# Performance work log

Hardware: AMD Instinct MI355X
Metric: run time of the kernel (lower is better)

## Reference

```python
import jax, jax.numpy as jnp
import numpy as np

N_COND, K, D = 16, 512, 256
B, H, W = 32, 64, 64


def setup_inputs() -> dict:
    key = jax.random.key(0)
    k1, k2, k3 = jax.random.split(key, 3)
    z_e_x = jax.random.normal(k1, (B, D, H, W), dtype=jnp.float32)
    C = jax.random.randint(k2, (B,), 0, N_COND, dtype=jnp.int64)
    bound = 1.0 / (K * N_COND)
    weight = jax.random.uniform(k3, (N_COND, K, D), dtype=jnp.float32,
                                minval=-bound, maxval=bound)
    return {"z_e_x": z_e_x, "C": C, "weight": weight}


def reference(z_e_x, C, weight):
    b, d, h, w = z_e_x.shape
    # [B, H, W, D] -> [B, N, D] with N = H*W
    z = jnp.transpose(z_e_x, (0, 2, 3, 1)).reshape(b, h * w, d)
    cb = weight[C]  # per-sample codebook [B, K, D] (batched gather replaces python loop)
    # squared euclidean distances: ||z||^2 - 2 z.e + ||e||^2  -> [B, N, K]
    dist = (jnp.sum(z * z, axis=-1, keepdims=True)
            - 2.0 * jnp.einsum('bnd,bkd->bnk', z, cb)
            + jnp.sum(cb * cb, axis=-1)[:, None, :])
    idx = jnp.argmin(dist, axis=-1)  # [B, N]
    quant = jnp.take_along_axis(cb, idx[..., None], axis=1)  # [B, N, D]
    # straight-through output (vq_st): forward = quantized
    z_q = z + jax.lax.stop_gradient(quant - z)
    # z_q_x_bar: plain gather from (non-detached) codebook
    z_q_bar = quant
    z_q_x = jnp.transpose(z_q.reshape(b, h, w, d), (0, 3, 1, 2))
    z_q_x_bar = jnp.transpose(z_q_bar.reshape(b, h, w, d), (0, 3, 1, 2))
    return z_q_x, z_q_x_bar
```

## Files before the change

kernel.cpp:

```cpp
#include <hip/hip_runtime.h>
#include <cfloat>

#define NB    32
#define ND    256
#define NK    512
#define NCOND 16
#define NHW   4096
#define PXT   64
#define MARGIN 1.3e-4f
#define QCAP  16

typedef __attribute__((ext_vector_type(8))) short bf16x8;
typedef __attribute__((ext_vector_type(4))) float f32x4;

__device__ __forceinline__ int loadC(const int* __restrict__ C, int b) {
  int orodd = 0;
#pragma unroll
  for (int i = 1; i < 32; i += 2) orodd |= C[i];
  return (orodd == 0) ? C[2 * b] : C[b];
}

__device__ __forceinline__ unsigned short rne_bf16(float x) {
  unsigned u = __float_as_uint(x);
  u += 0x7fffu + ((u >> 16) & 1u);
  return (unsigned short)(u >> 16);
}

__device__ float np_score_g(const float* __restrict__ z, size_t zoff,
                            const float* __restrict__ er, float S) {
  float P0 = 0.f, P1 = 0.f, P2 = 0.f, P3 = 0.f;
  for (int ch = 0; ch < 16; ++ch) {
    const float* eb = er + ch * 16;
    float4 e0 = *(const float4*)(eb + 0);
    float4 e1 = *(const float4*)(eb + 4);
    float4 e2 = *(const float4*)(eb + 8);
    float4 e3 = *(const float4*)(eb + 12);
    float zb[16];
#pragma unroll
    for (int q = 0; q < 16; ++q)
      zb[q] = z[zoff + (size_t)(ch * 16 + q) * NHW];
    P0 = __fadd_rn(P0, __fmul_rn(zb[12], e3.x));
    P0 = __fadd_rn(P0, __fmul_rn(zb[8],  e2.x));
    P0 = __fadd_rn(P0, __fmul_rn(zb[4],  e1.x));
    P0 = __fadd_rn(P0, __fmul_rn(zb[0],  e0.x));
    P1 = __fadd_rn(P1, __fmul_rn(zb[13], e3.y));
    P1 = __fadd_rn(P1, __fmul_rn(zb[9],  e2.y));
    P1 = __fadd_rn(P1, __fmul_rn(zb[5],  e1.y));
    P1 = __fadd_rn(P1, __fmul_rn(zb[1],  e0.y));
    P2 = __fadd_rn(P2, __fmul_rn(zb[14], e3.z));
    P2 = __fadd_rn(P2, __fmul_rn(zb[10], e2.z));
    P2 = __fadd_rn(P2, __fmul_rn(zb[6],  e1.z));
    P2 = __fadd_rn(P2, __fmul_rn(zb[2],  e0.z));
    P3 = __fadd_rn(P3, __fmul_rn(zb[15], e3.w));
    P3 = __fadd_rn(P3, __fmul_rn(zb[11], e2.w));
    P3 = __fadd_rn(P3, __fmul_rn(zb[7],  e1.w));
    P3 = __fadd_rn(P3, __fmul_rn(zb[3],  e0.w));
  }
  float G = __fadd_rn(__fadd_rn(P0, P1), __fadd_rn(P2, P3));
  return __fadd_rn(S, __fmul_rn(-2.0f, G));
}

__global__ __launch_bounds__(256) void k_split(
    const float* __restrict__ w, unsigned short* __restrict__ whi) {
  int i = (blockIdx.x * 256 + threadIdx.x) * 4;
  float4 v = *(const float4*)&w[i];
  int ci = i >> 17, rem = i & 131071;
  int code = rem >> 8, d = rem & 255;
  int dst = (ci << 17) + ((d >> 5) << 14) + (code << 5) + (d & 31);
  ushort4 h;
  h.x = rne_bf16(v.x); h.y = rne_bf16(v.y);
  h.z = rne_bf16(v.z); h.w = rne_bf16(v.w);
  *(ushort4*)&whi[dst] = h;
}

__device__ __forceinline__ int zofs(int px, int chunk) {
  return px * 256 + ((chunk ^ (px & 7)) * 8);
}

template <int PRE>
__global__ __launch_bounds__(512, 4) void k_vq(
    const float* __restrict__ z, const int* __restrict__ Cc,
    const float* __restrict__ w, const unsigned short* __restrict__ whi,
    float* __restrict__ out) {
  __shared__ __align__(16) unsigned short Zh[PXT * ND];
  __shared__ __align__(16) unsigned short Zl[PXT * ND];
  __shared__ float Ssh[PXT];
  __shared__ float Wmin[8][32];
  __shared__ float Thr[PXT];
  __shared__ int   qcnt[PXT], KB[PXT];
  __shared__ int   qk[PXT][QCAP];

  int orig = blockIdx.x;
  int blk  = (orig & 7) * 256 + (orig >> 3);
  int b    = blk >> 6;
  int n0   = (blk & 63) * PXT;
  int c    = loadC(Cc, b);
  int t    = threadIdx.x;
  int lane = t & 63;
  int wv   = t >> 6;
  int mw   = wv >> 2;
  int nw   = wv & 3;

  if (t < PXT) qcnt[t] = 0;

  const size_t zab = (size_t)b * ND * NHW;
  const size_t cbu = (size_t)c * (NK * ND);
  const int ar0  = mw * 32 + (lane & 15);
  const int koff = (lane >> 4) * 8;

  {
    int px = t & 63, dg = t >> 6;
    const float* zp = z + zab + n0 + px;
#pragma unroll
    for (int cc4 = 0; cc4 < 4; ++cc4) {
      int chunk = dg * 4 + cc4;
      bf16x8 h, l;
#pragma unroll
      for (int j = 0; j < 8; ++j) {
        float v = zp[(size_t)(chunk * 8 + j) * NHW];
        unsigned u = __float_as_uint(v) & 0xffff0000u;
        h[j] = (short)(u >> 16);
        l[j] = (short)rne_bf16(v - __uint_as_float(u));
      }
      *(bf16x8*)&Zh[zofs(px, chunk)] = h;
      *(bf16x8*)&Zl[zofs(px, chunk)] = l;
    }
  }

  {
    int spx = t >> 3, sj = t & 7;
    size_t sb = zab + n0 + spx;
    float r0 = 0.f, r1 = 0.f;
#pragma unroll
    for (int i = 0; i < 16; ++i) {
      float v0 = z[sb + (size_t)(8 * i + sj) * NHW];
      float v1 = z[sb + (size_t)(128 + 8 * i + sj) * NHW];
      r0 = __fadd_rn(r0, __fmul_rn(v0, v0));
      r1 = __fadd_rn(r1, __fmul_rn(v1, v1));
    }
#pragma unroll
    for (int off = 1; off < 8; off <<= 1) {
      r0 = __fadd_rn(r0, __shfl_xor(r0, off));
      r1 = __fadd_rn(r1, __shfl_xor(r1, off));
    }
    if (sj == 0) Ssh[spx] = __fadd_rn(r0, r1);
  }
  __syncthreads();

  f32x4 acc0[8], acc1[8];
#pragma unroll
  for (int nt = 0; nt < 8; ++nt) {
    acc0[nt] = (f32x4){0.f, 0.f, 0.f, 0.f};
    acc1[nt] = (f32x4){0.f, 0.f, 0.f, 0.f};
  }

#pragma unroll 1
  for (int ks = 0; ks < 8; ++ks) {
    int chunkA = ks * 4 + (lane >> 4);
    bf16x8 ah0 = *(const bf16x8*)&Zh[zofs(ar0,      chunkA)];
    bf16x8 al0 = *(const bf16x8*)&Zl[zofs(ar0,      chunkA)];
    bf16x8 ah1 = *(const bf16x8*)&Zh[zofs(ar0 + 16, chunkA)];
    bf16x8 al1 = *(const bf16x8*)&Zl[zofs(ar0 + 16, chunkA)];
#pragma unroll
    for (int nt = 0; nt < 8; ++nt) {
      int code = nw * 128 + nt * 16 + (lane & 15);
      bf16x8 bh;
      if constexpr (PRE) {
        bh = *(const bf16x8*)(whi + cbu + ks * (NK * 32) + code * 32 + koff);
      } else {
        const float* sf = w + ((size_t)c * NK + code) * ND + ks * 32 + koff;
        float4 f0 = *(const float4*)sf;
        float4 f1 = *(const float4*)(sf + 4);
        float xs[8] = {f0.x, f0.y, f0.z, f0.w, f1.x, f1.y, f1.z, f1.w};
#pragma unroll
        for (int q = 0; q < 8; ++q) bh[q] = (short)rne_bf16(xs[q]);
      }
      acc0[nt] = __builtin_amdgcn_mfma_f32_16x16x32_bf16(ah0, bh, acc0[nt], 0, 0, 0);
      acc0[nt] = __builtin_amdgcn_mfma_f32_16x16x32_bf16(al0, bh, acc0[nt], 0, 0, 0);
      acc1[nt] = __builtin_amdgcn_mfma_f32_16x16x32_bf16(ah1, bh, acc1[nt], 0, 0, 0);
      acc1[nt] = __builtin_amdgcn_mfma_f32_16x16x32_bf16(al1, bh, acc1[nt], 0, 0, 0);
    }
  }

  float pmin0[4], pmin1[4], S40[4], S41[4];
#pragma unroll
  for (int r = 0; r < 4; ++r) {
    int pr = mw * 32 + (lane >> 4) * 4 + r;
    S40[r] = Ssh[pr];
    S41[r] = Ssh[pr + 16];
    pmin0[r] = FLT_MAX; pmin1[r] = FLT_MAX;
  }
#pragma unroll
  for (int nt = 0; nt < 8; ++nt)
#pragma unroll
    for (int r = 0; r < 4; ++r) {
      float X0 = __fadd_rn(S40[r], __fmul_rn(-2.0f, acc0[nt][r]));
      float X1 = __fadd_rn(S41[r], __fmul_rn(-2.0f, acc1[nt][r]));
      acc0[nt][r] = X0; acc1[nt][r] = X1;
      pmin0[r] = fminf(pmin0[r], X0);
      pmin1[r] = fminf(pmin1[r], X1);
    }
#pragma unroll
  for (int r = 0; r < 4; ++r)
#pragma unroll
    for (int off = 1; off < 16; off <<= 1) {
      pmin0[r] = fminf(pmin0[r], __shfl_xor(pmin0[r], off));
      pmin1[r] = fminf(pmin1[r], __shfl_xor(pmin1[r], off));
    }
  if ((lane & 15) == 0) {
#pragma unroll
    for (int r = 0; r < 4; ++r) {
      Wmin[wv][(lane >> 4) * 4 + r]      = pmin0[r];
      Wmin[wv][16 + (lane >> 4) * 4 + r] = pmin1[r];
    }
  }
  __syncthreads();
  if (t < PXT) {
    int m2 = (t >> 5) * 4, i = t & 31;
    Thr[t] = fminf(fminf(Wmin[m2][i], Wmin[m2 + 1][i]),
                   fminf(Wmin[m2 + 2][i], Wmin[m2 + 3][i])) + MARGIN;
  }
  __syncthreads();

#pragma unroll
  for (int r = 0; r < 4; ++r) {
    int px0 = mw * 32 + (lane >> 4) * 4 + r;
    float th0 = Thr[px0], th1 = Thr[px0 + 16];
#pragma unroll
    for (int nt = 0; nt < 8; ++nt) {
      int kcode = nw * 128 + nt * 16 + (lane & 15);
      if (acc0[nt][r] <= th0) {
        int slot = atomicAdd(&qcnt[px0], 1);
        if (slot < QCAP) qk[px0][slot] = kcode;
      }
      if (acc1[nt][r] <= th1) {
        int slot = atomicAdd(&qcnt[px0 + 16], 1);
        if (slot < QCAP) qk[px0 + 16][slot] = kcode;
      }
    }
  }
  __syncthreads();

  {
    int px  = wv * 8 + (lane >> 3);
    int cnt = qcnt[px]; cnt = cnt < QCAP ? cnt : QCAP;
    float S = Ssh[px];
    size_t zoff = zab + n0 + px;
    float bv = FLT_MAX; int bk = 0x7fffffff;
#pragma unroll
    for (int m = 0; m < 2; ++m) {
      int slot = (lane & 7) + 8 * m;
      if (__any(slot < cnt)) {
        if (slot < cnt) {
          int k = qk[px][slot];
          float v = np_score_g(z, zoff, w + ((size_t)c * NK + k) * ND, S);
          if (v < bv || (v == bv && k < bk)) { bv = v; bk = k; }
        }
      }
    }
#pragma unroll
    for (int off = 1; off < 8; off <<= 1) {
      float ov = __shfl_xor(bv, off);
      int   ok = __shfl_xor(bk, off);
      if (ov < bv || (ov == bv && ok < bk)) { bv = ov; bk = ok; }
    }
    if ((lane & 7) == 0) KB[px] = bk;
  }
  __syncthreads();

  {
    int px = t & 63, dg = t >> 6;
    int kidx = KB[px];
    const float* er = w + ((size_t)c * NK + kidx) * ND;
    const size_t OUT2 = (size_t)NB * ND * NHW;
    size_t base = zab + n0 + px;
#pragma unroll
    for (int j = 0; j < 32; ++j) {
      int d = dg * 32 + j;
      float q  = er[d];
      float zv = z[base + (size_t)d * NHW];
      out[base + (size_t)d * NHW]        = __fadd_rn(zv, __fsub_rn(q, zv));
      out[base + (size_t)d * NHW + OUT2] = q;
    }
  }
}

extern "C" void kernel_launch(void* const* d_in, const int* in_sizes, int n_in,
                              void* d_out, int out_size, void* d_ws, size_t ws_size,
                              hipStream_t stream) {
  const float* z = (const float*)d_in[0];
  const int*   C = (const int*)d_in[1];
  const float* w = (const float*)d_in[2];
  float* out = (float*)d_out;

  const size_t NWEL = (size_t)NCOND * NK * ND;
  unsigned short* whi = (unsigned short*)d_ws;
  bool pre = ws_size >= NWEL * sizeof(unsigned short);

  if (pre) {
    k_split<<<(int)(NWEL / 1024), 256, 0, stream>>>(w, whi);
    k_vq<1><<<NB * (NHW / PXT), 512, 0, stream>>>(z, C, w, whi, out);
  } else {
    k_vq<0><<<NB * (NHW / PXT), 512, 0, stream>>>(z, C, w, whi, out);
  }
}
```

Before: 233.2 us.

## Split VQ kernel into score and gather kernels, skip rescoring single candidates

Moves the output writing out of the score kernel into a separate gather kernel launched with 256 threads, which reads the codebook row with float4 loads. Indices pass between the two kernels through a workspace buffer. The squared-norm computation now reduces through shared memory instead of shuffles. The refinement pass no longer rescores pixels that have only one candidate. The split lowers register and LDS pressure in the score kernel and frees the store phase from its occupancy limits, at the cost of an extra launch, an index round trip and reading z again. The fallback path now uses the workspace for indices, so it needs workspace memory it did not need before.

```diff
diff --git a/kernel.cpp b/kernel.cpp
--- a/kernel.cpp
+++ b/kernel.cpp
@@ -78,10 +78,10 @@
 }
 
 template <int PRE>
-__global__ __launch_bounds__(512, 4) void k_vq(
+__global__ __launch_bounds__(512, 4) void k_score(
     const float* __restrict__ z, const int* __restrict__ Cc,
     const float* __restrict__ w, const unsigned short* __restrict__ whi,
-    float* __restrict__ out) {
+    int* __restrict__ idxOut) {
   __shared__ __align__(16) unsigned short Zh[PXT * ND];
   __shared__ __align__(16) unsigned short Zl[PXT * ND];
   __shared__ float Ssh[PXT];
@@ -89,6 +89,8 @@
   __shared__ float Thr[PXT];
   __shared__ int   qcnt[PXT], KB[PXT];
   __shared__ int   qk[PXT][QCAP];
+
+  float* Rsh = (float*)qk;
 
   int orig = blockIdx.x;
   int blk  = (orig & 7) * 256 + (orig >> 3);
@@ -101,8 +103,6 @@
   int mw   = wv >> 2;
   int nw   = wv & 3;
 
-  if (t < PXT) qcnt[t] = 0;
-
   const size_t zab = (size_t)b * ND * NHW;
   const size_t cbu = (size_t)c * (NK * ND);
   const int ar0  = mw * 32 + (lane & 15);
@@ -128,22 +128,38 @@
   }
 
   {
-    int spx = t >> 3, sj = t & 7;
-    size_t sb = zab + n0 + spx;
-    float r0 = 0.f, r1 = 0.f;
-#pragma unroll
-    for (int i = 0; i < 16; ++i) {
-      float v0 = z[sb + (size_t)(8 * i + sj) * NHW];
-      float v1 = z[sb + (size_t)(128 + 8 * i + sj) * NHW];
+    int px = lane, j = wv;
+    const float* zp = z + zab + n0 + px;
+    float a0 = zp[(size_t)j * NHW];
+    float r0 = __fmul_rn(a0, a0);
+    float a1 = zp[(size_t)(128 + j) * NHW];
+    float r1 = __fmul_rn(a1, a1);
+#pragma unroll
+    for (int i = 1; i < 16; ++i) {
+      float v0 = zp[(size_t)(8 * i + j) * NHW];
       r0 = __fadd_rn(r0, __fmul_rn(v0, v0));
+      float v1 = zp[(size_t)(128 + 8 * i + j) * NHW];
       r1 = __fadd_rn(r1, __fmul_rn(v1, v1));
     }
-#pragma unroll
-    for (int off = 1; off < 8; off <<= 1) {
-      r0 = __fadd_rn(r0, __shfl_xor(r0, off));
-      r1 = __fadd_rn(r1, __shfl_xor(r1, off));
-    }
-    if (sj == 0) Ssh[spx] = __fadd_rn(r0, r1);
+    Rsh[j * 64 + px]       = r0;
+    Rsh[512 + j * 64 + px] = r1;
+  }
+  if (t < PXT) qcnt[t] = 0;
+  __syncthreads();
+
+  if (t < PXT) {
+    int px = t;
+    float pw0 = __fadd_rn(
+        __fadd_rn(__fadd_rn(Rsh[0 * 64 + px], Rsh[1 * 64 + px]),
+                  __fadd_rn(Rsh[2 * 64 + px], Rsh[3 * 64 + px])),
+        __fadd_rn(__fadd_rn(Rsh[4 * 64 + px], Rsh[5 * 64 + px]),
+                  __fadd_rn(Rsh[6 * 64 + px], Rsh[7 * 64 + px])));
+    float pw1 = __fadd_rn(
+        __fadd_rn(__fadd_rn(Rsh[512 + 0 * 64 + px], Rsh[512 + 1 * 64 + px]),
+                  __fadd_rn(Rsh[512 + 2 * 64 + px], Rsh[512 + 3 * 64 + px])),
+        __fadd_rn(__fadd_rn(Rsh[512 + 4 * 64 + px], Rsh[512 + 5 * 64 + px]),
+                  __fadd_rn(Rsh[512 + 6 * 64 + px], Rsh[512 + 7 * 64 + px])));
+    Ssh[px] = __fadd_rn(pw0, pw1);
   }
   __syncthreads();
 
@@ -247,14 +263,20 @@
     float S = Ssh[px];
     size_t zoff = zab + n0 + px;
     float bv = FLT_MAX; int bk = 0x7fffffff;
-#pragma unroll
-    for (int m = 0; m < 2; ++m) {
-      int slot = (lane & 7) + 8 * m;
-      if (__any(slot < cnt)) {
-        if (slot < cnt) {
-          int k = qk[px][slot];
-          float v = np_score_g(z, zoff, w + ((size_t)c * NK + k) * ND, S);
-          if (v < bv || (v == bv && k < bk)) { bv = v; bk = k; }
+    int slot0 = lane & 7;
+    if (cnt == 1) {
+      if (slot0 == 0) { bv = 0.f; bk = qk[px][0]; }
+    } else {
+#pragma unroll
+      for (int m = 0; m < 2; ++m) {
+        int slot = slot0 + 8 * m;
+        bool act = (cnt > 1) && (slot < cnt);
+        if (__any(act)) {
+          if (act) {
+            int k = qk[px][slot];
+            float v = np_score_g(z, zoff, w + ((size_t)c * NK + k) * ND, S);
+            if (v < bv || (v == bv && k < bk)) { bv = v; bk = k; }
+          }
         }
       }
     }
@@ -264,23 +286,39 @@
       int   ok = __shfl_xor(bk, off);
       if (ov < bv || (ov == bv && ok < bk)) { bv = ov; bk = ok; }
     }
-    if ((lane & 7) == 0) KB[px] = bk;
-  }
-  __syncthreads();
-
-  {
-    int px = t & 63, dg = t >> 6;
-    int kidx = KB[px];
-    const float* er = w + ((size_t)c * NK + kidx) * ND;
-    const size_t OUT2 = (size_t)NB * ND * NHW;
-    size_t base = zab + n0 + px;
-#pragma unroll
-    for (int j = 0; j < 32; ++j) {
-      int d = dg * 32 + j;
-      float q  = er[d];
+    if (slot0 == 0) KB[px] = bk;
+  }
+  __syncthreads();
+
+  if (t < PXT) idxOut[b * NHW + n0 + t] = KB[t];
+}
+
+__global__ __launch_bounds__(256) void k_gather(
+    const float* __restrict__ z, const int* __restrict__ Cc,
+    const float* __restrict__ w, const int* __restrict__ idx,
+    float* __restrict__ out) {
+  int orig = blockIdx.x;
+  int blk  = (orig & 7) * 256 + (orig >> 3);
+  int b    = blk >> 6;
+  int n0   = (blk & 63) * PXT;
+  int c    = loadC(Cc, b);
+  int t    = threadIdx.x;
+  int px   = t & 63, q = t >> 6;
+  int kidx = idx[b * NHW + n0 + px];
+  const float* er = w + ((size_t)c * NK + kidx) * ND + q * 64;
+  const size_t OUT2 = (size_t)NB * ND * NHW;
+  size_t base = (size_t)b * ND * NHW + n0 + px;
+#pragma unroll
+  for (int j4 = 0; j4 < 16; ++j4) {
+    float4 e4 = *(const float4*)(er + j4 * 4);
+    float ev[4] = {e4.x, e4.y, e4.z, e4.w};
+#pragma unroll
+    for (int jj = 0; jj < 4; ++jj) {
+      int d = q * 64 + j4 * 4 + jj;
+      float qv = ev[jj];
       float zv = z[base + (size_t)d * NHW];
-      out[base + (size_t)d * NHW]        = __fadd_rn(zv, __fsub_rn(q, zv));
-      out[base + (size_t)d * NHW + OUT2] = q;
+      out[base + (size_t)d * NHW]        = __fadd_rn(zv, __fsub_rn(qv, zv));
+      out[base + (size_t)d * NHW + OUT2] = qv;
     }
   }
 }
@@ -294,13 +332,19 @@
   float* out = (float*)d_out;
 
   const size_t NWEL = (size_t)NCOND * NK * ND;
-  unsigned short* whi = (unsigned short*)d_ws;
-  bool pre = ws_size >= NWEL * sizeof(unsigned short);
+  const size_t WHI_BYTES = NWEL * sizeof(unsigned short);
+  const size_t IDX_BYTES = (size_t)NB * NHW * sizeof(int);
+  bool pre = ws_size >= WHI_BYTES + IDX_BYTES;
 
   if (pre) {
+    unsigned short* whi = (unsigned short*)d_ws;
+    int* idx = (int*)((char*)d_ws + WHI_BYTES);
     k_split<<<(int)(NWEL / 1024), 256, 0, stream>>>(w, whi);
-    k_vq<1><<<NB * (NHW / PXT), 512, 0, stream>>>(z, C, w, whi, out);
+    k_score<1><<<NB * (NHW / PXT), 512, 0, stream>>>(z, C, w, whi, idx);
+    k_gather<<<NB * (NHW / PXT), 256, 0, stream>>>(z, C, w, idx, out);
   } else {
-    k_vq<0><<<NB * (NHW / PXT), 512, 0, stream>>>(z, C, w, whi, out);
-  }
-}
+    int* idx = (int*)d_ws;
+    k_score<0><<<NB * (NHW / PXT), 512, 0, stream>>>(z, C, w, nullptr, idx);
+    k_gather<<<NB * (NHW / PXT), 256, 0, stream>>>(z, C, w, idx, out);
+  }
+}
```

Measured after the change: 254.8 us. +9.3%, slower.
